# Optimization experiments

Measured on AMD Instinct MI355X. Metric: run time of the kernel, lower is better.

## Reference

```python
import jax, jax.numpy as jnp
import numpy as np

COST_CLASS = 2.0
COST_BBOX = 5.0
COST_GIOU = 2.0
ALPHA = 0.25
GAMMA = 2.0
INVALID_COST = 1.0e9


def _cxcywh_to_xyxy(b):
    cx, cy, w, h = b[..., 0], b[..., 1], b[..., 2], b[..., 3]
    return jnp.stack([cx - 0.5 * w, cy - 0.5 * h, cx + 0.5 * w, cy + 0.5 * h], axis=-1)


def _pairwise_giou(b1, b2):
    # b1: [B,Q,4] xyxy, b2: [B,T,4] xyxy -> giou [B,Q,T]
    area1 = (b1[..., 2] - b1[..., 0]) * (b1[..., 3] - b1[..., 1])  # [B,Q]
    area2 = (b2[..., 2] - b2[..., 0]) * (b2[..., 3] - b2[..., 1])  # [B,T]
    lt = jnp.maximum(b1[:, :, None, :2], b2[:, None, :, :2])  # [B,Q,T,2]
    rb = jnp.minimum(b1[:, :, None, 2:], b2[:, None, :, 2:])
    wh = jnp.clip(rb - lt, 0.0)
    inter = wh[..., 0] * wh[..., 1]  # [B,Q,T]
    union = area1[:, :, None] + area2[:, None, :] - inter
    iou = inter / union
    lt_e = jnp.minimum(b1[:, :, None, :2], b2[:, None, :, :2])
    rb_e = jnp.maximum(b1[:, :, None, 2:], b2[:, None, :, 2:])
    wh_e = jnp.clip(rb_e - lt_e, 0.0)
    area_e = wh_e[..., 0] * wh_e[..., 1]
    return iou - (area_e - union) / area_e


def setup_inputs() -> dict:
    key = jax.random.key(0)
    k1, k2, k3, k4 = jax.random.split(key, 4)
    B, Q, T = 32, 1800, 500
    pred_logits = jax.random.normal(k1, (B, Q, 1), dtype=jnp.float32)
    pred_boxes = jax.random.uniform(k2, (B, Q, 4), dtype=jnp.float32)
    boxes_padded = jax.random.uniform(k3, (B, T, 4), dtype=jnp.float32)
    num_boxes = jax.random.randint(k4, (B,), 1, T + 1, dtype=jnp.int64 if jax.config.read('jax_enable_x64') else jnp.int32)
    return {"pred_logits": pred_logits, "pred_boxes": pred_boxes,
            "boxes_padded": boxes_padded, "num_boxes": num_boxes}


def reference(pred_logits, pred_boxes, boxes_padded, num_boxes):
    out_score = pred_logits[..., 0]  # [B,Q]
    # L1 pairwise box distance (cdist p=1): [B,Q,T]
    cost_bbox = jnp.sum(jnp.abs(pred_boxes[:, :, None, :] - boxes_padded[:, None, :, :]), axis=-1)
    # GIoU cost
    cost_giou = -_pairwise_giou(_cxcywh_to_xyxy(pred_boxes), _cxcywh_to_xyxy(boxes_padded))
    # Focal (non-stable) classification cost, per-query then broadcast over T
    p = jax.nn.sigmoid(out_score)
    log_p = jax.nn.log_sigmoid(out_score)
    log_1mp = jax.nn.log_sigmoid(-out_score)
    cost_class = -ALPHA * (1.0 - p) ** GAMMA * log_p + (1.0 - ALPHA) * p ** GAMMA * log_1mp  # [B,Q]
    C = COST_BBOX * cost_bbox + COST_CLASS * cost_class[:, :, None] + COST_GIOU * cost_giou
    # Mask out padded (invalid) targets, mirroring C[i, :, :num_boxes[i]] slicing
    T = boxes_padded.shape[1]
    tgt_valid = jnp.arange(T)[None, :] < num_boxes[:, None]  # [B,T]
    C = jnp.where(tgt_valid[:, None, :], C, INVALID_COST)
    return C
```

## Files before the change

### kernel.cpp

```cpp
#include <hip/hip_runtime.h>


#define K_COST_CLASS 2.0f
#define K_COST_BBOX  5.0f
#define K_COST_GIOU  2.0f
#define K_ALPHA      0.25f
#define K_INVALID    1.0e9f

constexpr int B = 32;
constexpr int Q = 1800;
constexpr int T = 500;

__global__ __launch_bounds__(128) void matcher_cost_kernel(
    const float* __restrict__ pred_logits,
    const float* __restrict__ pred_boxes,
    const float* __restrict__ boxes_padded,
    const int*   __restrict__ num_boxes,
    float* __restrict__ out)
{
    const int bq  = blockIdx.x;
    const int b   = bq / Q;
    const int tid = threadIdx.x;

    const int t0 = tid * 4;
    if (t0 >= T) return;

    const float4 pb = *reinterpret_cast<const float4*>(pred_boxes + (size_t)bq * 4);
    const float pcx = pb.x, pcy = pb.y, pw = pb.z, ph = pb.w;
    const float px0 = __builtin_fmaf(-0.5f, pw, pcx);
    const float py0 = __builtin_fmaf(-0.5f, ph, pcy);
    const float px1 = __builtin_fmaf( 0.5f, pw, pcx);
    const float py1 = __builtin_fmaf( 0.5f, ph, pcy);
    const float parea = pw * ph;

    const float s = pred_logits[bq];
    const float e_na = __expf(-fabsf(s));
    const float lse  = __logf(1.f + e_na);
    const float log_p   = fminf(s, 0.f) - lse;
    const float log_1mp = fminf(-s, 0.f) - lse;
    const float r1pe = __builtin_amdgcn_rcpf(1.f + e_na);
    const float p    = (s >= 0.f) ? r1pe : e_na * r1pe;
    const float omp  = 1.f - p;
    const float cls_term = K_COST_CLASS *
        (-K_ALPHA * omp * omp * log_p + (1.f - K_ALPHA) * p * p * log_1mp);

    const int nb = num_boxes[b];

    const float4* tb_base =
        reinterpret_cast<const float4*>(boxes_padded + ((size_t)b * T + t0) * 4);

    float r[4];
#pragma unroll
    for (int j = 0; j < 4; ++j) {
        const int t = t0 + j;
        const float4 tb = tb_base[j];
        const float tcx = tb.x, tcy = tb.y, tw = tb.z, th = tb.w;

        const float cb = fabsf(pcx - tcx) + fabsf(pcy - tcy)
                       + fabsf(pw - tw)  + fabsf(ph - th);

        const float tx0 = __builtin_fmaf(-0.5f, tw, tcx);
        const float ty0 = __builtin_fmaf(-0.5f, th, tcy);
        const float tx1 = __builtin_fmaf( 0.5f, tw, tcx);
        const float ty1 = __builtin_fmaf( 0.5f, th, tcy);
        const float tarea = tw * th;

        const float iw = fmaxf(fminf(px1, tx1) - fmaxf(px0, tx0), 0.f);
        const float ih = fmaxf(fminf(py1, ty1) - fmaxf(py0, ty0), 0.f);
        const float inter = iw * ih;
        const float uni   = parea + tarea - inter;
        const float iou   = inter * __builtin_amdgcn_rcpf(uni);

        const float ew = fmaxf(px1, tx1) - fminf(px0, tx0);
        const float eh = fmaxf(py1, ty1) - fminf(py0, ty0);
        const float earea = ew * eh;
        const float giou  = iou - (earea - uni) * __builtin_amdgcn_rcpf(earea);

        const float c = __builtin_fmaf(K_COST_BBOX, cb,
                        __builtin_fmaf(-K_COST_GIOU, giou, cls_term));
        r[j] = (t < nb) ? c : K_INVALID;
    }

    float4 res = make_float4(r[0], r[1], r[2], r[3]);
    reinterpret_cast<float4*>(out + (size_t)bq * T)[tid] = res;
}

extern "C" void kernel_launch(void* const* d_in, const int* in_sizes, int n_in,
                              void* d_out, int out_size, void* d_ws, size_t ws_size,
                              hipStream_t stream) {
    const float* pred_logits  = (const float*)d_in[0];
    const float* pred_boxes   = (const float*)d_in[1];
    const float* boxes_padded = (const float*)d_in[2];
    const int*   num_boxes    = (const int*)d_in[3];
    float* out = (float*)d_out;

    dim3 grid(B * Q);
    dim3 block(128);
    matcher_cost_kernel<<<grid, block, 0, stream>>>(
        pred_logits, pred_boxes, boxes_padded, num_boxes, out);
}
```

Measured before the change: 150.7 us.

## Precompute per-query terms and reuse target boxes across query chunks

Adds a prepass kernel that computes per-query box corners, area and focal class cost once into workspace. The main kernel now has each block handle 25 queries for one batch, loads target boxes once into registers, and loops over queries reading the precomputed terms. The two reciprocals in GIoU are merged into one. The output write (~115 MB) still dominates, so the gain depends mostly on fewer blocks and less redundant work, at the cost of an extra launch and fewer, longer blocks.

```diff
diff --git a/kernel.cpp b/kernel.cpp
--- a/kernel.cpp
+++ b/kernel.cpp
@@ -10,22 +10,18 @@
 constexpr int B = 32;
 constexpr int Q = 1800;
 constexpr int T = 500;
+constexpr int QCHUNK = 25;
+constexpr int PSTRIDE = 16;
 
-__global__ __launch_bounds__(128) void matcher_cost_kernel(
+__global__ __launch_bounds__(256) void precompute_pred(
     const float* __restrict__ pred_logits,
     const float* __restrict__ pred_boxes,
-    const float* __restrict__ boxes_padded,
-    const int*   __restrict__ num_boxes,
-    float* __restrict__ out)
+    float* __restrict__ P)
 {
-    const int bq  = blockIdx.x;
-    const int b   = bq / Q;
-    const int tid = threadIdx.x;
+    const int i = blockIdx.x * 256 + threadIdx.x;
+    if (i >= B * Q) return;
 
-    const int t0 = tid * 4;
-    if (t0 >= T) return;
-
-    const float4 pb = *reinterpret_cast<const float4*>(pred_boxes + (size_t)bq * 4);
+    const float4 pb = *reinterpret_cast<const float4*>(pred_boxes + (size_t)i * 4);
     const float pcx = pb.x, pcy = pb.y, pw = pb.z, ph = pb.w;
     const float px0 = __builtin_fmaf(-0.5f, pw, pcx);
     const float py0 = __builtin_fmaf(-0.5f, ph, pcy);
@@ -33,7 +29,7 @@
     const float py1 = __builtin_fmaf( 0.5f, ph, pcy);
     const float parea = pw * ph;
 
-    const float s = pred_logits[bq];
+    const float s = pred_logits[i];
     const float e_na = __expf(-fabsf(s));
     const float lse  = __logf(1.f + e_na);
     const float log_p   = fminf(s, 0.f) - lse;
@@ -44,45 +40,77 @@
     const float cls_term = K_COST_CLASS *
         (-K_ALPHA * omp * omp * log_p + (1.f - K_ALPHA) * p * p * log_1mp);
 
+    float4* o = reinterpret_cast<float4*>(P + (size_t)i * PSTRIDE);
+    o[0] = make_float4(px0, py0, px1, py1);
+    o[1] = make_float4(pcx, pcy, pw, ph);
+    o[2] = make_float4(parea, cls_term, 0.f, 0.f);
+}
+
+__global__ __launch_bounds__(128) void matcher_cost_kernel(
+    const float* __restrict__ boxes_padded,
+    const int*   __restrict__ num_boxes,
+    const float* __restrict__ P,
+    float* __restrict__ out)
+{
+    const int b  = blockIdx.y;
+    const int q0 = blockIdx.x * QCHUNK;
+    const int tid = threadIdx.x;
+    const int t0  = tid * 4;
+    if (t0 >= T) return;
+
     const int nb = num_boxes[b];
 
     const float4* tb_base =
         reinterpret_cast<const float4*>(boxes_padded + ((size_t)b * T + t0) * 4);
-
-    float r[4];
+    float tcx[4], tcy[4], tw_[4], th_[4];
+    float tx0[4], ty0[4], tx1[4], ty1[4], tarea[4];
+    bool  valid[4];
 #pragma unroll
     for (int j = 0; j < 4; ++j) {
-        const int t = t0 + j;
         const float4 tb = tb_base[j];
-        const float tcx = tb.x, tcy = tb.y, tw = tb.z, th = tb.w;
-
-        const float cb = fabsf(pcx - tcx) + fabsf(pcy - tcy)
-                       + fabsf(pw - tw)  + fabsf(ph - th);
-
-        const float tx0 = __builtin_fmaf(-0.5f, tw, tcx);
-        const float ty0 = __builtin_fmaf(-0.5f, th, tcy);
-        const float tx1 = __builtin_fmaf( 0.5f, tw, tcx);
-        const float ty1 = __builtin_fmaf( 0.5f, th, tcy);
-        const float tarea = tw * th;
-
-        const float iw = fmaxf(fminf(px1, tx1) - fmaxf(px0, tx0), 0.f);
-        const float ih = fmaxf(fminf(py1, ty1) - fmaxf(py0, ty0), 0.f);
-        const float inter = iw * ih;
-        const float uni   = parea + tarea - inter;
-        const float iou   = inter * __builtin_amdgcn_rcpf(uni);
-
-        const float ew = fmaxf(px1, tx1) - fminf(px0, tx0);
-        const float eh = fmaxf(py1, ty1) - fminf(py0, ty0);
-        const float earea = ew * eh;
-        const float giou  = iou - (earea - uni) * __builtin_amdgcn_rcpf(earea);
-
-        const float c = __builtin_fmaf(K_COST_BBOX, cb,
-                        __builtin_fmaf(-K_COST_GIOU, giou, cls_term));
-        r[j] = (t < nb) ? c : K_INVALID;
+        tcx[j] = tb.x; tcy[j] = tb.y; tw_[j] = tb.z; th_[j] = tb.w;
+        tx0[j] = __builtin_fmaf(-0.5f, tb.z, tb.x);
+        ty0[j] = __builtin_fmaf(-0.5f, tb.w, tb.y);
+        tx1[j] = __builtin_fmaf( 0.5f, tb.z, tb.x);
+        ty1[j] = __builtin_fmaf( 0.5f, tb.w, tb.y);
+        tarea[j] = tb.z * tb.w;
+        valid[j] = (t0 + j) < nb;
     }
 
-    float4 res = make_float4(r[0], r[1], r[2], r[3]);
-    reinterpret_cast<float4*>(out + (size_t)bq * T)[tid] = res;
+    float4* orow0 = reinterpret_cast<float4*>(out + ((size_t)b * Q + q0) * T);
+
+#pragma unroll 2
+    for (int qi = 0; qi < QCHUNK; ++qi) {
+        const float* p = P + ((size_t)b * Q + (q0 + qi)) * PSTRIDE;
+        const float px0 = p[0], py0 = p[1], px1 = p[2], py1 = p[3];
+        const float pcx = p[4], pcy = p[5], pw = p[6], ph = p[7];
+        const float parea = p[8], cls_term = p[9];
+
+        float r[4];
+#pragma unroll
+        for (int j = 0; j < 4; ++j) {
+            const float cb = fabsf(pcx - tcx[j]) + fabsf(pcy - tcy[j])
+                           + fabsf(pw - tw_[j]) + fabsf(ph - th_[j]);
+
+            const float iw = fmaxf(fminf(px1, tx1[j]) - fmaxf(px0, tx0[j]), 0.f);
+            const float ih = fmaxf(fminf(py1, ty1[j]) - fmaxf(py0, ty0[j]), 0.f);
+            const float inter = iw * ih;
+            const float uni   = (parea + tarea[j]) - inter;
+
+            const float ew = fmaxf(px1, tx1[j]) - fminf(px0, tx0[j]);
+            const float eh = fmaxf(py1, ty1[j]) - fminf(py0, ty0[j]);
+            const float earea = ew * eh;
+
+            const float num    = __builtin_fmaf(earea, inter - uni, uni * uni);
+            const float rdenom = __builtin_amdgcn_rcpf(uni * earea);
+            const float giou   = num * rdenom;
+
+            const float c = __builtin_fmaf(K_COST_BBOX, cb,
+                            __builtin_fmaf(-K_COST_GIOU, giou, cls_term));
+            r[j] = valid[j] ? c : K_INVALID;
+        }
+        orow0[(size_t)qi * (T / 4) + tid] = make_float4(r[0], r[1], r[2], r[3]);
+    }
 }
 
 extern "C" void kernel_launch(void* const* d_in, const int* in_sizes, int n_in,
@@ -93,9 +121,12 @@
     const float* boxes_padded = (const float*)d_in[2];
     const int*   num_boxes    = (const int*)d_in[3];
     float* out = (float*)d_out;
+    float* P   = (float*)d_ws;
 
-    dim3 grid(B * Q);
-    dim3 block(128);
-    matcher_cost_kernel<<<grid, block, 0, stream>>>(
-        pred_logits, pred_boxes, boxes_padded, num_boxes, out);
+    precompute_pred<<<dim3((B * Q + 255) / 256), dim3(256), 0, stream>>>(
+        pred_logits, pred_boxes, P);
+
+    dim3 grid(Q / QCHUNK, B);
+    matcher_cost_kernel<<<grid, dim3(128), 0, stream>>>(
+        boxes_padded, num_boxes, P, out);
 }
```

After: 144.3 us. 4.3% less time.
